# Performance work log

Measured on AMD Instinct MI355X. Metric: run time of the kernel, lower is better.

## Reference

```python
import jax, jax.numpy as jnp
import numpy as np

D_MODEL = 1024
EXPAND = 2
D_INNER = D_MODEL * EXPAND
KERNEL = 4
EPS = 1e-5


def setup_inputs() -> dict:
    key = jax.random.key(0)
    ks = jax.random.split(key, 8)
    B, L = 2, 4096
    x = jax.random.normal(ks[0], (B, L, D_MODEL), dtype=jnp.float32)
    norm_w = jnp.ones((D_MODEL,), jnp.float32)
    norm_b = jnp.zeros((D_MODEL,), jnp.float32)
    # torch Linear weight layout [out, in]
    in_proj_w = jax.random.normal(ks[1], (2 * D_INNER, D_MODEL), jnp.float32) / np.sqrt(D_MODEL)
    # depthwise Conv1d weight [d_inner, 1, K]
    conv_w = jax.random.normal(ks[2], (D_INNER, 1, KERNEL), jnp.float32) / np.sqrt(KERNEL)
    conv_b = jax.random.normal(ks[3], (D_INNER,), jnp.float32) * 0.02
    gate_w = jax.random.normal(ks[4], (D_INNER, D_INNER), jnp.float32) / np.sqrt(D_INNER)
    gate_b = jnp.zeros((D_INNER,), jnp.float32)
    out_proj_w = jax.random.normal(ks[5], (D_MODEL, D_INNER), jnp.float32) / np.sqrt(D_INNER)
    return {"x": x, "norm_w": norm_w, "norm_b": norm_b, "in_proj_w": in_proj_w,
            "conv_w": conv_w, "conv_b": conv_b, "gate_w": gate_w, "gate_b": gate_b,
            "out_proj_w": out_proj_w}


def _layernorm(x, w, b):
    mu = jnp.mean(x, axis=-1, keepdims=True)
    var = jnp.var(x, axis=-1, keepdims=True)
    return (x - mu) * jax.lax.rsqrt(var + EPS) * w + b


def _glru(x, norm_w, norm_b, in_proj_w, conv_w, conv_b, gate_w, gate_b, out_proj_w):
    B, L, D = x.shape
    residual = x
    xn = _layernorm(x, norm_w, norm_b)
    xz = jnp.einsum('bld,ed->ble', xn, in_proj_w)  # [B,L,2*d_inner]
    x_inner, z = jnp.split(xz, 2, axis=-1)
    # causal depthwise conv: torch pads 3 both sides then slices [:L] == left-pad 3
    lhs = jnp.transpose(x_inner, (0, 2, 1))  # [B, C, L]
    conv = jax.lax.conv_general_dilated(
        lhs, conv_w, window_strides=(1,), padding=[(KERNEL - 1, 0)],
        feature_group_count=D_INNER,
        dimension_numbers=('NCH', 'OIH', 'NCH'))
    x_conv = jnp.transpose(conv, (0, 2, 1)) + conv_b  # [B, L, C]
    x_conv = jax.nn.silu(x_conv)
    a = jax.nn.sigmoid(jnp.einsum('blc,ec->ble', x_conv, gate_w) + gate_b)
    b = (1.0 - a) * x_conv
    # h_t = a_t * h_{t-1} + b_t, h_0 prior = 0 -> parallel associative scan
    def combine(e1, e2):
        a1, b1 = e1
        a2, b2 = e2
        return a1 * a2, a2 * b1 + b2
    _, y = jax.lax.associative_scan(combine, (a, b), axis=1)
    y = y * jax.nn.silu(z)
    return residual + jnp.einsum('blc,dc->bld', y, out_proj_w)


def reference(x, norm_w, norm_b, in_proj_w, conv_w, conv_b, gate_w, gate_b, out_proj_w):
    return _glru(x, norm_w, norm_b, in_proj_w, conv_w, conv_b, gate_w, gate_b, out_proj_w)
```

## Files before the change

kernel.cpp:

```cpp
#include <hip/hip_runtime.h>
#include <cstdint>

#define D_MODEL 1024
#define D_INNER 2048
#define LSEQ    4096
#define BATCH   2
#define M_ROWS  (BATCH * LSEQ)
#define CHUNK   128
#define NCHUNK  (LSEQ / CHUNK)

typedef unsigned short u16;
typedef __bf16 bf16x8 __attribute__((ext_vector_type(8)));
typedef float f32x4 __attribute__((ext_vector_type(4)));
typedef u16 u16x4 __attribute__((ext_vector_type(4)));

__device__ __forceinline__ u16 f2bf(float f) {
  union { float f; unsigned u; } x; x.f = f;
  unsigned u = x.u;
  unsigned r = (u + 0x7FFFu + ((u >> 16) & 1u)) >> 16;
  return (u16)r;
}
__device__ __forceinline__ float bf2f(u16 h) {
  union { unsigned u; float f; } x; x.u = ((unsigned)h) << 16;
  return x.f;
}
__device__ __forceinline__ float sigmoidf_(float v) { return 1.0f / (1.0f + expf(-v)); }
__device__ __forceinline__ float siluf_(float v)    { return v / (1.0f + expf(-v)); }

__device__ __forceinline__ void gl_lds16(const void* g, void* l) {
  __builtin_amdgcn_global_load_lds(
      (const __attribute__((address_space(1))) void*)g,
      (__attribute__((address_space(3))) void*)l, 16, 0, 0);
}

#define SBAR()   asm volatile("s_barrier" ::: "memory")
#define WAITV0() asm volatile("s_waitcnt vmcnt(0)" ::: "memory")
#define SGB()    __builtin_amdgcn_sched_barrier(0)

__global__ void __launch_bounds__(256)
cast3_kernel(const float* __restrict__ w0, const float* __restrict__ w1,
             const float* __restrict__ w2, u16* __restrict__ o0,
             u16* __restrict__ o1, u16* __restrict__ o2) {
  const int n04 = 2 * D_INNER * D_MODEL / 4;
  const int n14 = D_INNER * D_INNER / 4;
  const int n24 = D_MODEL * D_INNER / 4;
  int i = blockIdx.x * 256 + threadIdx.x;
  const float* src; u16* dst; int j;
  if (i < n04)            { src = w0; dst = o0; j = i; }
  else if (i < n04 + n14) { src = w1; dst = o1; j = i - n04; }
  else if (i < n04 + n14 + n24) { src = w2; dst = o2; j = i - n04 - n14; }
  else return;
  float4 v = ((const float4*)src)[j];
  u16x4 o;
  o.x = f2bf(v.x); o.y = f2bf(v.y); o.z = f2bf(v.z); o.w = f2bf(v.w);
  ((u16x4*)dst)[j] = o;
}

__global__ void __launch_bounds__(256)
ln_kernel(const float* __restrict__ x, const float* __restrict__ w,
          const float* __restrict__ b, u16* __restrict__ xn) {
  const int row = blockIdx.x;
  const int t = threadIdx.x;
  const float4 v = ((const float4*)(x + (size_t)row * D_MODEL))[t];
  float s  = v.x + v.y + v.z + v.w;
  float ss = v.x * v.x + v.y * v.y + v.z * v.z + v.w * v.w;
#pragma unroll
  for (int o = 32; o > 0; o >>= 1) {
    s  += __shfl_xor(s, o);
    ss += __shfl_xor(ss, o);
  }
  __shared__ float red[8];
  const int wid = t >> 6, lane = t & 63;
  if (lane == 0) { red[wid] = s; red[4 + wid] = ss; }
  __syncthreads();
  s  = red[0] + red[1] + red[2] + red[3];
  ss = red[4] + red[5] + red[6] + red[7];
  const float mu  = s * (1.0f / D_MODEL);
  const float var = ss * (1.0f / D_MODEL) - mu * mu;
  const float rs  = rsqrtf(var + 1e-5f);
  const float4 wv = ((const float4*)w)[t];
  const float4 bv = ((const float4*)b)[t];
  u16x4 o4;
  o4.x = f2bf((v.x - mu) * rs * wv.x + bv.x);
  o4.y = f2bf((v.y - mu) * rs * wv.y + bv.y);
  o4.z = f2bf((v.z - mu) * rs * wv.z + bv.z);
  o4.w = f2bf((v.w - mu) * rs * wv.w + bv.w);
  ((u16x4*)(xn + (size_t)row * D_MODEL))[t] = o4;
}

#define MFMA_BF16 __builtin_amdgcn_mfma_f32_16x16x32_bf16

template<int EPI, int BN>
__global__ void __launch_bounds__(512, 2)
gemmP(const u16* __restrict__ A, const u16* __restrict__ Bm,
      int M, int N, int K,
      const float* __restrict__ ef, float* __restrict__ of,
      u16* __restrict__ ob0, u16* __restrict__ ob1) {
  constexpr int NF  = BN / 64;
  constexpr int NF2 = NF / 2;
  constexpr int BBY = BN * 128;
  constexpr int BH  = BN / 128;
  __shared__ __align__(1024) char lds[65536 + 2 * BBY];
  const int tid = threadIdx.x, wid = tid >> 6, lane = tid & 63;
  const int nbx = N / BN;
  const int nwg = nbx * (M >> 8);
  const int bid = blockIdx.x;
  const int cpx = nwg >> 3;
  const int swzb = (bid & 7) * cpx + (bid >> 3);
  const int bx = swzb % nbx, by = swzb / nbx;
  const size_t m0 = (size_t)by << 8;
  const size_t n0 = (size_t)bx * BN;
  const int wr = wid >> 2, wc = wid & 3;
  const size_t rb = (size_t)K * 2;

  const int strow = lane >> 3;
  const int stchk = (lane & 7) ^ strow;
  const char* gA = (const char*)A  + (m0 + (size_t)(wid * 8 + strow)) * rb + stchk * 16;
  const char* gB = (const char*)Bm + (n0 + (size_t)(wid * 8 + strow)) * rb + stchk * 16;
  const int sdw = wid * 1024;

  auto ST_A = [&](int t) {
    char* d = lds + (t & 1) * 32768 + sdw;
    const char* s = gA + (size_t)t * 128;
#pragma unroll
    for (int h = 0; h < 2; ++h) {
      gl_lds16(s + (size_t)(h * 128) * rb,      d + h * 16384);
      gl_lds16(s + (size_t)(h * 128 + 64) * rb, d + h * 16384 + 8192);
    }
  };
  auto ST_B = [&](int t) {
    char* d = lds + 65536 + (t & 1) * BBY + sdw;
    const char* s = gB + (size_t)t * 128;
#pragma unroll
    for (int h = 0; h < BH; ++h) {
      gl_lds16(s + (size_t)(h * 128) * rb,      d + h * 16384);
      gl_lds16(s + (size_t)(h * 128 + 64) * rb, d + h * 16384 + 8192);
    }
  };

  const int q = lane >> 4, r15 = lane & 15;
  const int kx0 = ((q ^ (r15 & 7)) << 4);
  const int kx1 = (((4 + q) ^ (r15 & 7)) << 4);
  const int arow = r15 * 128;
  const int bwoff = (BN == 256) ? ((wc >> 1) * 16384) : 0;
  const int brow  = (BN == 256) ? (((wc & 1) * 64 + r15) * 128)
                                : ((wc * 32 + r15) * 128);

  bf16x8 af0[8], af1[8], b01[NF2], b23[NF2], c01[NF2], c23[NF2];
  f32x4 acc[8][NF] = {};

#define RDA(dst, kx, base) _Pragma("unroll") \
  for (int mf = 0; mf < 8; ++mf) dst[mf] = *(const bf16x8*)((base) + mf * 2048 + arow + (kx));
#define RDB(dst, kx, base, nf0) _Pragma("unroll") \
  for (int nf = 0; nf < NF2; ++nf) dst[nf] = *(const bf16x8*)((base) + (nf0 + nf) * 2048 + brow + (kx));
#define MM(afr, bfr, nf0) do { __builtin_amdgcn_s_setprio(1); _Pragma("unroll") \
  for (int mf = 0; mf < 8; ++mf) _Pragma("unroll") \
    for (int nf = 0; nf < NF2; ++nf) \
      acc[mf][nf0 + nf] = MFMA_BF16(afr[mf], bfr[nf], acc[mf][nf0 + nf], 0, 0, 0); \
  __builtin_amdgcn_s_setprio(0); } while (0)

  const int nk = K >> 6;

  ST_A(0); ST_B(0);
  WAITV0();
  SBAR();
  {
    const char* Ab = lds + wr * 16384;
    const char* Bb = lds + 65536 + bwoff;
    RDA(af0, kx0, Ab);
    RDB(b01, kx0, Bb, 0);
  }

  for (int t = 0; t < nk; ++t) {
    const int p = t & 1;
    const char* Ab = lds + p * 32768 + wr * 16384;
    const char* Bb = lds + 65536 + p * BBY + bwoff;
    const char* An = lds + (p ^ 1) * 32768 + wr * 16384;
    const char* Bn = lds + 65536 + (p ^ 1) * BBY + bwoff;
    const bool pf = (t + 1 < nk);

    if (pf) ST_A(t + 1);
    RDB(b23, kx0, Bb, NF2);
    SGB();
    MM(af0, b01, 0);
    SGB();

    if (pf) ST_B(t + 1);
    RDA(af1, kx1, Ab);
    RDB(c01, kx1, Bb, 0);
    SGB();
    MM(af0, b23, NF2);
    SGB();

    RDB(c23, kx1, Bb, NF2);
    SGB();
    MM(af1, c01, 0);
    SGB();

    MM(af1, c23, NF2);
    if (pf) {
      WAITV0();
      SBAR();
      RDA(af0, kx0, An);
      RDB(b01, kx0, Bn, 0);
    }
  }

#undef RDA
#undef RDB
#undef MM

  const int c0 = lane & 15;
  const int r0 = (lane >> 4) << 2;
  const bool isz = (EPI == 0) && (n0 >= (size_t)D_INNER);
#pragma unroll
  for (int mf = 0; mf < 8; ++mf) {
#pragma unroll
    for (int nf = 0; nf < NF; ++nf) {
#pragma unroll
      for (int rg = 0; rg < 4; ++rg) {
        const size_t row = m0 + (size_t)(wr * 128 + mf * 16 + r0 + rg);
        const size_t col = n0 + (size_t)(wc * (BN / 4) + nf * 16 + c0);
        const float v = acc[mf][nf][rg];
        if (EPI == 0) {
          if (!isz) ob0[row * D_INNER + col] = f2bf(v);
          else      ob1[row * D_INNER + (col - D_INNER)] = f2bf(siluf_(v));
        } else if (EPI == 1) {
          ob0[row * (size_t)N + col] = f2bf(v);
        } else {
          of[row * (size_t)N + col] = v + ef[row * (size_t)N + col];
        }
      }
    }
  }
}

__global__ void __launch_bounds__(256)
conv_silu_kernel(const u16* __restrict__ xin, const float* __restrict__ cw,
                 const float* __restrict__ cb, u16* __restrict__ xc) {
  const int c   = blockIdx.x * 256 + threadIdx.x;
  const int l0  = blockIdx.y * 8;
  const int bat = blockIdx.z;
  const size_t base = ((size_t)bat * LSEQ) * D_INNER + c;
  const float w0 = cw[c * 4 + 0], w1 = cw[c * 4 + 1], w2 = cw[c * 4 + 2], w3 = cw[c * 4 + 3];
  const float bb = cb[c];
  float v[11];
#pragma unroll
  for (int i = 0; i < 11; ++i) {
    const int l = l0 - 3 + i;
    v[i] = (l >= 0) ? bf2f(xin[base + (size_t)l * D_INNER]) : 0.0f;
  }
#pragma unroll
  for (int r = 0; r < 8; ++r) {
    const float acc = bb + w0 * v[r] + w1 * v[r + 1] + w2 * v[r + 2] + w3 * v[r + 3];
    xc[base + (size_t)(l0 + r) * D_INNER] = f2bf(siluf_(acc));
  }
}

__global__ void __launch_bounds__(256)
scan_a_kernel(const u16* __restrict__ g, const u16* __restrict__ xc,
              const float* __restrict__ gbias,
              float* __restrict__ cA, float* __restrict__ cB) {
  const int c   = (blockIdx.x * 256 + threadIdx.x) * 2;
  const int ch  = blockIdx.y;
  const int bat = blockIdx.z;
  const float bb0 = gbias[c], bb1 = gbias[c + 1];
  size_t idx = ((size_t)bat * LSEQ + (size_t)ch * CHUNK) * D_INNER + c;
  float pA0 = 1.0f, hB0 = 0.0f, pA1 = 1.0f, hB1 = 0.0f;
  for (int t = 0; t < CHUNK; ++t) {
    const ushort2 gg = *(const ushort2*)(g + idx);
    const ushort2 xx = *(const ushort2*)(xc + idx);
    const float a0 = sigmoidf_(bf2f(gg.x) + bb0);
    const float a1 = sigmoidf_(bf2f(gg.y) + bb1);
    pA0 *= a0; hB0 = a0 * hB0 + (1.0f - a0) * bf2f(xx.x);
    pA1 *= a1; hB1 = a1 * hB1 + (1.0f - a1) * bf2f(xx.y);
    idx += D_INNER;
  }
  const size_t o = ((size_t)bat * NCHUNK + ch) * D_INNER + c;
  *(float2*)(cA + o) = make_float2(pA0, pA1);
  *(float2*)(cB + o) = make_float2(hB0, hB1);
}

__global__ void __launch_bounds__(256)
scan_b_kernel(const float* __restrict__ cA, const float* __restrict__ cB,
              float* __restrict__ carry) {
  const int tid = blockIdx.x * 256 + threadIdx.x;
  const int bat = tid >> 11;
  const int c   = tid & (D_INNER - 1);
  float h = 0.0f;
  const size_t base = (size_t)bat * NCHUNK * D_INNER + c;
  for (int i = 0; i < NCHUNK; ++i) {
    const size_t o = base + (size_t)i * D_INNER;
    carry[o] = h;
    h = cA[o] * h + cB[o];
  }
}

__global__ void __launch_bounds__(256)
scan_c_kernel(const u16* __restrict__ g, const u16* __restrict__ xc,
              const u16* __restrict__ sz, const float* __restrict__ gbias,
              const float* __restrict__ carry, u16* __restrict__ yg) {
  const int c   = (blockIdx.x * 256 + threadIdx.x) * 2;
  const int ch  = blockIdx.y;
  const int bat = blockIdx.z;
  const float bb0 = gbias[c], bb1 = gbias[c + 1];
  const float2 h2 = *(const float2*)(carry + ((size_t)bat * NCHUNK + ch) * D_INNER + c);
  float h0 = h2.x, h1 = h2.y;
  size_t idx = ((size_t)bat * LSEQ + (size_t)ch * CHUNK) * D_INNER + c;
  for (int t = 0; t < CHUNK; ++t) {
    const ushort2 gg = *(const ushort2*)(g + idx);
    const ushort2 xx = *(const ushort2*)(xc + idx);
    const ushort2 zz = *(const ushort2*)(sz + idx);
    const float a0 = sigmoidf_(bf2f(gg.x) + bb0);
    const float a1 = sigmoidf_(bf2f(gg.y) + bb1);
    h0 = a0 * h0 + (1.0f - a0) * bf2f(xx.x);
    h1 = a1 * h1 + (1.0f - a1) * bf2f(xx.y);
    ushort2 o2;
    o2.x = f2bf(h0 * bf2f(zz.x));
    o2.y = f2bf(h1 * bf2f(zz.y));
    *(ushort2*)(yg + idx) = o2;
    idx += D_INNER;
  }
}

extern "C" void kernel_launch(void* const* d_in, const int* in_sizes, int n_in,
                              void* d_out, int out_size, void* d_ws, size_t ws_size,
                              hipStream_t stream) {
  const float* x         = (const float*)d_in[0];
  const float* norm_w    = (const float*)d_in[1];
  const float* norm_b    = (const float*)d_in[2];
  const float* in_proj_w = (const float*)d_in[3];
  const float* conv_w    = (const float*)d_in[4];
  const float* conv_b    = (const float*)d_in[5];
  const float* gate_w    = (const float*)d_in[6];
  const float* gate_b    = (const float*)d_in[7];
  const float* out_proj_w= (const float*)d_in[8];
  float* out = (float*)d_out;

  char* p = (char*)d_ws;
  u16* xn      = (u16*)p; p += (size_t)M_ROWS * D_MODEL * 2;
  u16* w_in    = (u16*)p; p += (size_t)2 * D_INNER * D_MODEL * 2;
  u16* w_gate  = (u16*)p; p += (size_t)D_INNER * D_INNER * 2;
  u16* w_out   = (u16*)p; p += (size_t)D_MODEL * D_INNER * 2;
  u16* x_inner = (u16*)p; p += (size_t)M_ROWS * D_INNER * 2;
  u16* szb     = (u16*)p; p += (size_t)M_ROWS * D_INNER * 2;
  u16* xconv   = (u16*)p; p += (size_t)M_ROWS * D_INNER * 2;
  u16* gbuf    = (u16*)p; p += (size_t)M_ROWS * D_INNER * 2;
  u16* yg      = (u16*)p; p += (size_t)M_ROWS * D_INNER * 2;
  float* cA    = (float*)p; p += (size_t)BATCH * NCHUNK * D_INNER * 4;
  float* cB    = (float*)p; p += (size_t)BATCH * NCHUNK * D_INNER * 4;
  float* carry = (float*)p; p += (size_t)BATCH * NCHUNK * D_INNER * 4;
  if ((size_t)(p - (char*)d_ws) > ws_size) return;

  const int ncast4 = (2 * D_INNER * D_MODEL + D_INNER * D_INNER + D_MODEL * D_INNER) / 4;
  cast3_kernel<<<dim3((ncast4 + 255) / 256), 256, 0, stream>>>(
      in_proj_w, gate_w, out_proj_w, w_in, w_gate, w_out);

  ln_kernel<<<dim3(M_ROWS), 256, 0, stream>>>(x, norm_w, norm_b, xn);

  gemmP<0, 256><<<dim3((M_ROWS / 256) * (2 * D_INNER / 256)), 512, 0, stream>>>(
      xn, w_in, M_ROWS, 2 * D_INNER, D_MODEL, nullptr, nullptr, x_inner, szb);

  conv_silu_kernel<<<dim3(D_INNER / 256, LSEQ / 8, BATCH), 256, 0, stream>>>(x_inner, conv_w, conv_b, xconv);

  gemmP<1, 256><<<dim3((M_ROWS / 256) * (D_INNER / 256)), 512, 0, stream>>>(
      xconv, w_gate, M_ROWS, D_INNER, D_INNER, nullptr, nullptr, gbuf, nullptr);

  scan_a_kernel<<<dim3(D_INNER / 512, NCHUNK, BATCH), 256, 0, stream>>>(gbuf, xconv, gate_b, cA, cB);
  scan_b_kernel<<<dim3(BATCH * D_INNER / 256), 256, 0, stream>>>(cA, cB, carry);
  scan_c_kernel<<<dim3(D_INNER / 512, NCHUNK, BATCH), 256, 0, stream>>>(gbuf, xconv, szb, gate_b, carry, yg);

  gemmP<2, 128><<<dim3((M_ROWS / 256) * (D_MODEL / 128)), 512, 0, stream>>>(
      yg, w_out, M_ROWS, D_MODEL, D_INNER, x, out, nullptr, nullptr);
}
```

Measured before the change: 323.3 us.

## Split-K out_proj GEMM with bf16 partials and vectorize conv and scan kernels

Measured after the change: 381.0 us. 17.8% more time.

```diff
diff --git a/kernel.cpp b/kernel.cpp
--- a/kernel.cpp
+++ b/kernel.cpp
@@ -90,16 +90,13 @@
 
 #define MFMA_BF16 __builtin_amdgcn_mfma_f32_16x16x32_bf16
 
-template<int EPI, int BN>
+template<int EPI>
 __global__ void __launch_bounds__(512, 2)
 gemmP(const u16* __restrict__ A, const u16* __restrict__ Bm,
-      int M, int N, int K,
+      int M, int N, int K, int Kfull,
       const float* __restrict__ ef, float* __restrict__ of,
       u16* __restrict__ ob0, u16* __restrict__ ob1) {
-  constexpr int NF  = BN / 64;
-  constexpr int NF2 = NF / 2;
-  constexpr int BBY = BN * 128;
-  constexpr int BH  = BN / 128;
+  constexpr int BN = 256, NF = 4, NF2 = 2, BBY = BN * 128, BH = BN / 128;
   __shared__ __align__(1024) char lds[65536 + 2 * BBY];
   const int tid = threadIdx.x, wid = tid >> 6, lane = tid & 63;
   const int nbx = N / BN;
@@ -111,12 +108,13 @@
   const size_t m0 = (size_t)by << 8;
   const size_t n0 = (size_t)bx * BN;
   const int wr = wid >> 2, wc = wid & 3;
-  const size_t rb = (size_t)K * 2;
+  const size_t rb = (size_t)Kfull * 2;
+  const size_t kofs = (size_t)blockIdx.y * (size_t)K * 2;
 
   const int strow = lane >> 3;
   const int stchk = (lane & 7) ^ strow;
-  const char* gA = (const char*)A  + (m0 + (size_t)(wid * 8 + strow)) * rb + stchk * 16;
-  const char* gB = (const char*)Bm + (n0 + (size_t)(wid * 8 + strow)) * rb + stchk * 16;
+  const char* gA = (const char*)A  + (m0 + (size_t)(wid * 8 + strow)) * rb + stchk * 16 + kofs;
+  const char* gB = (const char*)Bm + (n0 + (size_t)(wid * 8 + strow)) * rb + stchk * 16 + kofs;
   const int sdw = wid * 1024;
 
   auto ST_A = [&](int t) {
@@ -142,9 +140,8 @@
   const int kx0 = ((q ^ (r15 & 7)) << 4);
   const int kx1 = (((4 + q) ^ (r15 & 7)) << 4);
   const int arow = r15 * 128;
-  const int bwoff = (BN == 256) ? ((wc >> 1) * 16384) : 0;
-  const int brow  = (BN == 256) ? (((wc & 1) * 64 + r15) * 128)
-                                : ((wc * 32 + r15) * 128);
+  const int bwoff = (wc >> 1) * 16384;
+  const int brow  = ((wc & 1) * 64 + r15) * 128;
 
   bf16x8 af0[8], af1[8], b01[NF2], b23[NF2], c01[NF2], c23[NF2];
   f32x4 acc[8][NF] = {};
@@ -213,6 +210,7 @@
   const int c0 = lane & 15;
   const int r0 = (lane >> 4) << 2;
   const bool isz = (EPI == 0) && (n0 >= (size_t)D_INNER);
+  u16* ob0p = (EPI == 1) ? (ob0 + (size_t)blockIdx.y * (size_t)M * N) : ob0;
 #pragma unroll
   for (int mf = 0; mf < 8; ++mf) {
 #pragma unroll
@@ -220,13 +218,13 @@
 #pragma unroll
       for (int rg = 0; rg < 4; ++rg) {
         const size_t row = m0 + (size_t)(wr * 128 + mf * 16 + r0 + rg);
-        const size_t col = n0 + (size_t)(wc * (BN / 4) + nf * 16 + c0);
+        const size_t col = n0 + (size_t)(wc * 64 + nf * 16 + c0);
         const float v = acc[mf][nf][rg];
         if (EPI == 0) {
           if (!isz) ob0[row * D_INNER + col] = f2bf(v);
           else      ob1[row * D_INNER + (col - D_INNER)] = f2bf(siluf_(v));
         } else if (EPI == 1) {
-          ob0[row * (size_t)N + col] = f2bf(v);
+          ob0p[row * (size_t)N + col] = f2bf(v);
         } else {
           of[row * (size_t)N + col] = v + ef[row * (size_t)N + col];
         }
@@ -236,24 +234,58 @@
 }
 
 __global__ void __launch_bounds__(256)
+reduce3_kernel(const u16* __restrict__ part, const float* __restrict__ x,
+               float* __restrict__ out) {
+  const size_t MN = (size_t)M_ROWS * D_MODEL;
+  const size_t i = ((size_t)blockIdx.x * 256 + threadIdx.x) * 4;
+  const u16x4 a = *(const u16x4*)(part + i);
+  const u16x4 b = *(const u16x4*)(part + MN + i);
+  const float4 xv = *(const float4*)(x + i);
+  float4 o;
+  o.x = bf2f(a.x) + bf2f(b.x) + xv.x;
+  o.y = bf2f(a.y) + bf2f(b.y) + xv.y;
+  o.z = bf2f(a.z) + bf2f(b.z) + xv.z;
+  o.w = bf2f(a.w) + bf2f(b.w) + xv.w;
+  *(float4*)(out + i) = o;
+}
+
+__global__ void __launch_bounds__(256)
 conv_silu_kernel(const u16* __restrict__ xin, const float* __restrict__ cw,
                  const float* __restrict__ cb, u16* __restrict__ xc) {
-  const int c   = blockIdx.x * 256 + threadIdx.x;
+  const int c   = (blockIdx.x * 256 + threadIdx.x) * 4;
   const int l0  = blockIdx.y * 8;
   const int bat = blockIdx.z;
   const size_t base = ((size_t)bat * LSEQ) * D_INNER + c;
-  const float w0 = cw[c * 4 + 0], w1 = cw[c * 4 + 1], w2 = cw[c * 4 + 2], w3 = cw[c * 4 + 3];
-  const float bb = cb[c];
-  float v[11];
+  float4 w[4];
+#pragma unroll
+  for (int j = 0; j < 4; ++j) w[j] = ((const float4*)cw)[c + j];
+  const float4 bb = *(const float4*)(cb + c);
+  float v[11][4];
 #pragma unroll
   for (int i = 0; i < 11; ++i) {
     const int l = l0 - 3 + i;
-    v[i] = (l >= 0) ? bf2f(xin[base + (size_t)l * D_INNER]) : 0.0f;
-  }
+    if (l >= 0) {
+      const u16x4 u = *(const u16x4*)(xin + base + (size_t)l * D_INNER);
+      v[i][0] = bf2f(u.x); v[i][1] = bf2f(u.y); v[i][2] = bf2f(u.z); v[i][3] = bf2f(u.w);
+    } else {
+      v[i][0] = v[i][1] = v[i][2] = v[i][3] = 0.0f;
+    }
+  }
+  const float bba[4] = {bb.x, bb.y, bb.z, bb.w};
 #pragma unroll
   for (int r = 0; r < 8; ++r) {
-    const float acc = bb + w0 * v[r] + w1 * v[r + 1] + w2 * v[r + 2] + w3 * v[r + 3];
-    xc[base + (size_t)(l0 + r) * D_INNER] = f2bf(siluf_(acc));
+    u16x4 o;
+#pragma unroll
+    for (int j = 0; j < 4; ++j) {
+      const float acc = bba[j] + w[j].x * v[r][j] + w[j].y * v[r + 1][j]
+                      + w[j].z * v[r + 2][j] + w[j].w * v[r + 3][j];
+      const float sv = siluf_(acc);
+      if (j == 0) o.x = f2bf(sv);
+      else if (j == 1) o.y = f2bf(sv);
+      else if (j == 2) o.z = f2bf(sv);
+      else o.w = f2bf(sv);
+    }
+    *(u16x4*)(xc + base + (size_t)(l0 + r) * D_INNER) = o;
   }
 }
 
@@ -261,24 +293,30 @@
 scan_a_kernel(const u16* __restrict__ g, const u16* __restrict__ xc,
               const float* __restrict__ gbias,
               float* __restrict__ cA, float* __restrict__ cB) {
-  const int c   = (blockIdx.x * 256 + threadIdx.x) * 2;
+  const int c   = (blockIdx.x * 256 + threadIdx.x) * 4;
   const int ch  = blockIdx.y;
   const int bat = blockIdx.z;
-  const float bb0 = gbias[c], bb1 = gbias[c + 1];
+  const float4 bb = *(const float4*)(gbias + c);
+  const float bba[4] = {bb.x, bb.y, bb.z, bb.w};
   size_t idx = ((size_t)bat * LSEQ + (size_t)ch * CHUNK) * D_INNER + c;
-  float pA0 = 1.0f, hB0 = 0.0f, pA1 = 1.0f, hB1 = 0.0f;
+  float pA[4] = {1.0f, 1.0f, 1.0f, 1.0f};
+  float hB[4] = {0.0f, 0.0f, 0.0f, 0.0f};
   for (int t = 0; t < CHUNK; ++t) {
-    const ushort2 gg = *(const ushort2*)(g + idx);
-    const ushort2 xx = *(const ushort2*)(xc + idx);
-    const float a0 = sigmoidf_(bf2f(gg.x) + bb0);
-    const float a1 = sigmoidf_(bf2f(gg.y) + bb1);
-    pA0 *= a0; hB0 = a0 * hB0 + (1.0f - a0) * bf2f(xx.x);
-    pA1 *= a1; hB1 = a1 * hB1 + (1.0f - a1) * bf2f(xx.y);
+    const u16x4 gg = *(const u16x4*)(g + idx);
+    const u16x4 xx = *(const u16x4*)(xc + idx);
+    const float gv[4] = {bf2f(gg.x), bf2f(gg.y), bf2f(gg.z), bf2f(gg.w)};
+    const float xv[4] = {bf2f(xx.x), bf2f(xx.y), bf2f(xx.z), bf2f(xx.w)};
+#pragma unroll
+    for (int j = 0; j < 4; ++j) {
+      const float a = sigmoidf_(gv[j] + bba[j]);
+      pA[j] *= a;
+      hB[j] = a * hB[j] + (1.0f - a) * xv[j];
+    }
     idx += D_INNER;
   }
   const size_t o = ((size_t)bat * NCHUNK + ch) * D_INNER + c;
-  *(float2*)(cA + o) = make_float2(pA0, pA1);
-  *(float2*)(cB + o) = make_float2(hB0, hB1);
+  *(float4*)(cA + o) = make_float4(pA[0], pA[1], pA[2], pA[3]);
+  *(float4*)(cB + o) = make_float4(hB[0], hB[1], hB[2], hB[3]);
 }
 
 __global__ void __launch_bounds__(256)
@@ -300,25 +338,31 @@
 scan_c_kernel(const u16* __restrict__ g, const u16* __restrict__ xc,
               const u16* __restrict__ sz, const float* __restrict__ gbias,
               const float* __restrict__ carry, u16* __restrict__ yg) {
-  const int c   = (blockIdx.x * 256 + threadIdx.x) * 2;
+  const int c   = (blockIdx.x * 256 + threadIdx.x) * 4;
   const int ch  = blockIdx.y;
   const int bat = blockIdx.z;
-  const float bb0 = gbias[c], bb1 = gbias[c + 1];
-  const float2 h2 = *(const float2*)(carry + ((size_t)bat * NCHUNK + ch) * D_INNER + c);
-  float h0 = h2.x, h1 = h2.y;
+  const float4 bb = *(const float4*)(gbias + c);
+  const float bba[4] = {bb.x, bb.y, bb.z, bb.w};
+  const float4 h4 = *(const float4*)(carry + ((size_t)bat * NCHUNK + ch) * D_INNER + c);
+  float h[4] = {h4.x, h4.y, h4.z, h4.w};
   size_t idx = ((size_t)bat * LSEQ + (size_t)ch * CHUNK) * D_INNER + c;
   for (int t = 0; t < CHUNK; ++t) {
-    const ushort2 gg = *(const ushort2*)(g + idx);
-    const ushort2 xx = *(const ushort2*)(xc + idx);
-    const ushort2 zz = *(const ushort2*)(sz + idx);
-    const float a0 = sigmoidf_(bf2f(gg.x) + bb0);
-    const float a1 = sigmoidf_(bf2f(gg.y) + bb1);
-    h0 = a0 * h0 + (1.0f - a0) * bf2f(xx.x);
-    h1 = a1 * h1 + (1.0f - a1) * bf2f(xx.y);
-    ushort2 o2;
-    o2.x = f2bf(h0 * bf2f(zz.x));
-    o2.y = f2bf(h1 * bf2f(zz.y));
-    *(ushort2*)(yg + idx) = o2;
+    const u16x4 gg = *(const u16x4*)(g + idx);
+    const u16x4 xx = *(const u16x4*)(xc + idx);
+    const u16x4 zz = *(const u16x4*)(sz + idx);
+    const float gv[4] = {bf2f(gg.x), bf2f(gg.y), bf2f(gg.z), bf2f(gg.w)};
+    const float xv[4] = {bf2f(xx.x), bf2f(xx.y), bf2f(xx.z), bf2f(xx.w)};
+    const float zv[4] = {bf2f(zz.x), bf2f(zz.y), bf2f(zz.z), bf2f(zz.w)};
+    u16x4 o;
+#pragma unroll
+    for (int j = 0; j < 4; ++j) {
+      const float a = sigmoidf_(gv[j] + bba[j]);
+      h[j] = a * h[j] + (1.0f - a) * xv[j];
+      const u16 ob = f2bf(h[j] * zv[j]);
+      if (j == 0) o.x = ob; else if (j == 1) o.y = ob;
+      else if (j == 2) o.z = ob; else o.w = ob;
+    }
+    *(u16x4*)(yg + idx) = o;
     idx += D_INNER;
   }
 }
@@ -347,6 +391,7 @@
   u16* xconv   = (u16*)p; p += (size_t)M_ROWS * D_INNER * 2;
   u16* gbuf    = (u16*)p; p += (size_t)M_ROWS * D_INNER * 2;
   u16* yg      = (u16*)p; p += (size_t)M_ROWS * D_INNER * 2;
+  u16* part    = (u16*)p; p += (size_t)2 * M_ROWS * D_MODEL * 2;
   float* cA    = (float*)p; p += (size_t)BATCH * NCHUNK * D_INNER * 4;
   float* cB    = (float*)p; p += (size_t)BATCH * NCHUNK * D_INNER * 4;
   float* carry = (float*)p; p += (size_t)BATCH * NCHUNK * D_INNER * 4;
@@ -358,18 +403,21 @@
 
   ln_kernel<<<dim3(M_ROWS), 256, 0, stream>>>(x, norm_w, norm_b, xn);
 
-  gemmP<0, 256><<<dim3((M_ROWS / 256) * (2 * D_INNER / 256)), 512, 0, stream>>>(
-      xn, w_in, M_ROWS, 2 * D_INNER, D_MODEL, nullptr, nullptr, x_inner, szb);
-
-  conv_silu_kernel<<<dim3(D_INNER / 256, LSEQ / 8, BATCH), 256, 0, stream>>>(x_inner, conv_w, conv_b, xconv);
-
-  gemmP<1, 256><<<dim3((M_ROWS / 256) * (D_INNER / 256)), 512, 0, stream>>>(
-      xconv, w_gate, M_ROWS, D_INNER, D_INNER, nullptr, nullptr, gbuf, nullptr);
-
-  scan_a_kernel<<<dim3(D_INNER / 512, NCHUNK, BATCH), 256, 0, stream>>>(gbuf, xconv, gate_b, cA, cB);
+  gemmP<0><<<dim3((M_ROWS / 256) * (2 * D_INNER / 256)), 512, 0, stream>>>(
+      xn, w_in, M_ROWS, 2 * D_INNER, D_MODEL, D_MODEL, nullptr, nullptr, x_inner, szb);
+
+  conv_silu_kernel<<<dim3(D_INNER / 1024, LSEQ / 8, BATCH), 256, 0, stream>>>(
+      x_inner, conv_w, conv_b, xconv);
+
+  gemmP<1><<<dim3((M_ROWS / 256) * (D_INNER / 256)), 512, 0, stream>>>(
+      xconv, w_gate, M_ROWS, D_INNER, D_INNER, D_INNER, nullptr, nullptr, gbuf, nullptr);
+
+  scan_a_kernel<<<dim3(D_INNER / 1024, NCHUNK, BATCH), 256, 0, stream>>>(gbuf, xconv, gate_b, cA, cB);
   scan_b_kernel<<<dim3(BATCH * D_INNER / 256), 256, 0, stream>>>(cA, cB, carry);
-  scan_c_kernel<<<dim3(D_INNER / 512, NCHUNK, BATCH), 256, 0, stream>>>(gbuf, xconv, szb, gate_b, carry, yg);
-
-  gemmP<2, 128><<<dim3((M_ROWS / 256) * (D_MODEL / 128)), 512, 0, stream>>>(
-      yg, w_out, M_ROWS, D_MODEL, D_INNER, x, out, nullptr, nullptr);
-}
+  scan_c_kernel<<<dim3(D_INNER / 1024, NCHUNK, BATCH), 256, 0, stream>>>(gbuf, xconv, szb, gate_b, carry, yg);
+
+  gemmP<1><<<dim3((M_ROWS / 256) * (D_MODEL / 256), 2), 512, 0, stream>>>(
+      yg, w_out, M_ROWS, D_MODEL, D_INNER / 2, D_INNER, nullptr, nullptr, part, nullptr);
+
+  reduce3_kernel<<<dim3(M_ROWS * D_MODEL / 4 / 256), 256, 0, stream>>>(part, x, out);
+}
```
